# Kernel tuning notes

Hardware: AMD Instinct MI355X
Metric: run time of the kernel (lower is better)

The kernel has to match this reference:

```python
import jax, jax.numpy as jnp
import numpy as np

N = 65536          # number of points
K = 32             # max neighbors (padded)
C_IN = 64
C_OUT = 64
KERNEL = 27        # spatial filter bins (3x3x3)
MULT = 1           # depth multiplier
BN_EPS = 1e-5


def setup_inputs() -> dict:
    key = jax.random.key(0)
    ks = jax.random.split(key, 8)
    inputs = jax.random.normal(ks[0], (N, C_IN), dtype=jnp.float32)
    nn_count = jnp.maximum(jax.random.randint(ks[1], (N,), 0, K, dtype=jnp.int32), 1)
    nn_index = jax.random.randint(ks[2], (N, K), 0, N, dtype=jnp.int32)
    filt_index = jax.random.randint(ks[3], (N, K), 0, KERNEL, dtype=jnp.int32)
    # learned parameters (xavier-normal-ish init)
    sw_std = float(np.sqrt(2.0 / (KERNEL * C_IN + MULT)))
    spatial_weights = jax.random.normal(ks[4], (KERNEL, C_IN, MULT), dtype=jnp.float32) * sw_std
    dw_std = float(np.sqrt(2.0 / (C_IN * MULT + C_OUT)))
    depth_weights = jax.random.normal(ks[5], (C_IN * MULT, C_OUT), dtype=jnp.float32) * dw_std
    biases = jnp.zeros((1, C_OUT), dtype=jnp.float32)
    gamma = jnp.ones((C_OUT,), dtype=jnp.float32)
    beta = jnp.zeros((C_OUT,), dtype=jnp.float32)
    return {"inputs": inputs, "spatial_weights": spatial_weights,
            "depth_weights": depth_weights, "biases": biases,
            "gamma": gamma, "beta": beta,
            "nn_count": nn_count, "nn_index": nn_index, "filt_index": filt_index}


def reference(inputs, spatial_weights, depth_weights, biases, gamma, beta,
              nn_count, nn_index, filt_index):
    n, k = nn_index.shape
    # valid-neighbor mask for padded neighborhoods
    mask = (jnp.arange(k, dtype=jnp.int32)[None, :] < nn_count[:, None]).astype(inputs.dtype)  # [N,K]
    gathered = inputs[nn_index] * mask[:, :, None]            # [N,K,C]
    wg = spatial_weights[filt_index]                          # [N,K,C,M]
    # spatial filtering: average over valid neighbors with per-pair filter weights
    sp = jnp.einsum('nkc,nkcm->ncm', gathered, wg) / nn_count[:, None, None].astype(inputs.dtype)
    x = sp.reshape(n, -1) @ depth_weights + biases            # [N,C_OUT]
    x = jax.nn.relu(x)
    # BatchNorm1d (training mode: batch statistics, biased variance)
    mean = jnp.mean(x, axis=0)
    var = jnp.var(x, axis=0)
    out = gamma * (x - mean) * jax.lax.rsqrt(var + BN_EPS) + beta
    return out
```

## Files before the change

### kernel.cpp

```cpp
#include <hip/hip_runtime.h>
#include <math.h>

#define KMAX   32
#define CIN    64
#define COUT   64
#define NKERN  27
#define GPW    8
#define MMT    2
constexpr float BN_EPS = 1e-5f;

typedef _Float16 f16;
typedef _Float16 f16x2 __attribute__((ext_vector_type(2)));
typedef _Float16 f16x8 __attribute__((ext_vector_type(8)));
typedef float    f32x4 __attribute__((ext_vector_type(4)));

union h2i { f16x2 h; int i; };

__global__ __launch_bounds__(256) void k_cvtpack(
    const float* __restrict__ in,
    f16*         __restrict__ out,
    const float* __restrict__ dw,
    f16*         __restrict__ dwf,
    float*       __restrict__ stats,
    const int*   __restrict__ nn_count,
    const int*   __restrict__ nn_index,
    const int*   __restrict__ filt_index,
    int*         __restrict__ packed,
    float*       __restrict__ invc,
    int total4, int cvtBlocks, int total_q, int zrowIdx)
{
    const int bid = blockIdx.x;
    if (bid == 0) {
        const int t = threadIdx.x;
        if (t < 128) stats[t] = 0.0f;
        if (t < CIN) out[(size_t)zrowIdx * CIN + t] = (f16)0.0f;
        for (int i = t; i < 512; i += 256) {
            const int j = i >> 7, s = (i >> 6) & 1, l = i & 63;
            const int col = j * 16 + (l & 15);
            const int k0  = s * 32 + ((l >> 4) * 8);
            #pragma unroll
            for (int e = 0; e < 8; ++e)
                dwf[(size_t)i * 8 + e] = (f16)dw[(k0 + e) * COUT + col];
        }
    }
    if (bid < cvtBlocks) {
        const int stride = cvtBlocks * 256;
        for (int i = bid * 256 + threadIdx.x; i < total4; i += stride) {
            const float4 v = ((const float4*)in)[i];
            f16x2 a = { (f16)v.x, (f16)v.y };
            f16x2 b = { (f16)v.z, (f16)v.w };
            uint2 u;
            u.x = *(const unsigned int*)&a;
            u.y = *(const unsigned int*)&b;
            ((uint2*)out)[i] = u;
        }
    } else {
        const int t = (bid - cvtBlocks) * 256 + threadIdx.x;
        if (t < total_q) {
            const int n = t >> 3, q = t & 7;
            const int cnt = nn_count[n];
            const int4 ni = ((const int4*)nn_index)[t];
            const int4 fi = ((const int4*)filt_index)[t];
            const int k0 = q * 4;
            const int px = (((k0 + 0) < cnt ? ni.x : zrowIdx) << 7) | (fi.x << 25);
            const int py = (((k0 + 1) < cnt ? ni.y : zrowIdx) << 7) | (fi.y << 25);
            const int pz = (((k0 + 2) < cnt ? ni.z : zrowIdx) << 7) | (fi.z << 25);
            const int pw = (((k0 + 3) < cnt ? ni.w : zrowIdx) << 7) | (fi.w << 25);
            int* bp = packed + (size_t)n * KMAX;
            int2 ev = { px, pz };
            int2 od = { py, pw };
            *(int2*)(bp + 2 * q)      = ev;
            *(int2*)(bp + 16 + 2 * q) = od;
            if (q == 0) invc[n] = 1.0f / (float)cnt;
        }
    }
}

__global__ __launch_bounds__(256, 8) void k_gather(
    const f16*   __restrict__ gh,
    const float* __restrict__ sw,
    const int*   __restrict__ packed,
    const float* __restrict__ invc,
    f16*         __restrict__ sp)
{
    __shared__ f16 sw_lds[NKERN * CIN];
    const int tid = threadIdx.x;
    for (int i = tid; i < NKERN * CIN; i += 256) sw_lds[i] = (f16)sw[i];
    __syncthreads();

    const int wave = tid >> 6;
    const int lane = tid & 63;
    const int h    = lane >> 5;
    const unsigned cpos4 = (unsigned)(lane & 31) * 4;
    const int base = blockIdx.x * (4 * GPW) + wave * GPW;
    const char* __restrict__ ghb = (const char*)gh;
    const char* __restrict__ swb = (const char*)sw_lds;

    for (int p = 0; p < GPW; ++p) {
        const int n = base + p;
        const int4* __restrict__ pk4 =
            (const int4*)(packed + (size_t)n * KMAX + h * 16);

        int mypk[16];
        #pragma unroll
        for (int q = 0; q < 4; ++q) *(int4*)&mypk[4 * q] = pk4[q];
        const float ic = invc[n];

        f16x2 g2[16];
        #pragma unroll
        for (int i = 0; i < 16; ++i)
            g2[i] = *(const f16x2*)(ghb + (((unsigned)mypk[i] & 0xFFFFFFu) + cpos4));

        f16x2 a0 = {(f16)0.f, (f16)0.f}, a1 = a0, a2 = a0, a3 = a0;
        #pragma unroll
        for (int i = 0; i < 16; ++i) {
            const unsigned swoff = (((unsigned)mypk[i] >> 25) << 7) + cpos4;
            const f16x2 w2 = *(const f16x2*)(swb + swoff);
            f16x2& a = (i & 3) == 0 ? a0 : (i & 3) == 1 ? a1
                     : (i & 3) == 2 ? a2 : a3;
            a = __builtin_elementwise_fma(g2[i], w2, a);
        }
        f16x2 stot = (a0 + a1) + (a2 + a3);

        h2i cv; cv.h = stot;
        h2i ov; ov.i = __shfl_xor(cv.i, 32);
        stot = stot + ov.h;

        if (h == 0) {
            f16x2 res = { (f16)((float)stot.x * ic), (f16)((float)stot.y * ic) };
            *(f16x2*)(sp + (size_t)n * CIN + (cpos4 >> 1)) = res;
        }
    }
}

#define MM_LOAD_AB(r0)                                                        \
    const f16* arow = sp + (size_t)((r0) + (lane & 15)) * CIN + ((lane >> 4) * 8); \
    const f16x8 a0 = *(const f16x8*)(arow);                                   \
    const f16x8 a1 = *(const f16x8*)(arow + 32);

__global__ __launch_bounds__(256) void k_mm_stats(
    const f16*   __restrict__ sp,
    const f16*   __restrict__ dwf,
    const float* __restrict__ bias,
    float*       __restrict__ stats)
{
    __shared__ float rsum[4][4][16], rsq[4][4][16];
    const int tid = threadIdx.x;
    const int wave = tid >> 6, lane = tid & 63;

    const f16x8* dwf8 = (const f16x8*)dwf;
    f16x8 b[4][2];
    #pragma unroll
    for (int j = 0; j < 4; ++j) {
        b[j][0] = dwf8[(j * 2 + 0) * 64 + lane];
        b[j][1] = dwf8[(j * 2 + 1) * 64 + lane];
    }
    float bias_c[4];
    #pragma unroll
    for (int j = 0; j < 4; ++j) bias_c[j] = bias[j * 16 + (lane & 15)];

    float sum[4] = {0, 0, 0, 0}, sq[4] = {0, 0, 0, 0};
    const int rowbase = (blockIdx.x * 4 + wave) * (MMT * 16);

    for (int t = 0; t < MMT; ++t) {
        MM_LOAD_AB(rowbase + t * 16)
        #pragma unroll
        for (int j = 0; j < 4; ++j) {
            f32x4 acc = {0.f, 0.f, 0.f, 0.f};
            acc = __builtin_amdgcn_mfma_f32_16x16x32_f16(a0, b[j][0], acc, 0, 0, 0);
            acc = __builtin_amdgcn_mfma_f32_16x16x32_f16(a1, b[j][1], acc, 0, 0, 0);
            #pragma unroll
            for (int r = 0; r < 4; ++r) {
                const float x = fmaxf(acc[r] + bias_c[j], 0.0f);
                sum[j] += x;
                sq[j]  += x * x;
            }
        }
    }

    #pragma unroll
    for (int j = 0; j < 4; ++j) {
        sum[j] += __shfl_xor(sum[j], 16); sum[j] += __shfl_xor(sum[j], 32);
        sq[j]  += __shfl_xor(sq[j], 16);  sq[j]  += __shfl_xor(sq[j], 32);
    }
    if (lane < 16) {
        #pragma unroll
        for (int j = 0; j < 4; ++j) {
            rsum[wave][j][lane] = sum[j];
            rsq[wave][j][lane]  = sq[j];
        }
    }
    __syncthreads();
    if (wave == 0 && lane < 16) {
        #pragma unroll
        for (int j = 0; j < 4; ++j) {
            const float s = rsum[0][j][lane] + rsum[1][j][lane]
                          + rsum[2][j][lane] + rsum[3][j][lane];
            const float q = rsq[0][j][lane] + rsq[1][j][lane]
                          + rsq[2][j][lane] + rsq[3][j][lane];
            atomicAdd(&stats[j * 16 + lane], s);
            atomicAdd(&stats[COUT + j * 16 + lane], q);
        }
    }
}

__global__ void k_finalize(const float* __restrict__ stats,
                           const float* __restrict__ gamma,
                           const float* __restrict__ beta,
                           float* __restrict__ sc_sh, float invN) {
    const int j = threadIdx.x;
    const float mean = stats[j] * invN;
    const float var  = stats[COUT + j] * invN - mean * mean;
    const float s    = gamma[j] * rsqrtf(var + BN_EPS);
    sc_sh[j]        = s;
    sc_sh[COUT + j] = beta[j] - mean * s;
}

__global__ __launch_bounds__(256) void k_mm_out(
    const f16*   __restrict__ sp,
    const f16*   __restrict__ dwf,
    const float* __restrict__ bias,
    const float* __restrict__ sc_sh,
    float*       __restrict__ out)
{
    const int tid = threadIdx.x;
    const int wave = tid >> 6, lane = tid & 63;

    const f16x8* dwf8 = (const f16x8*)dwf;
    f16x8 b[4][2];
    #pragma unroll
    for (int j = 0; j < 4; ++j) {
        b[j][0] = dwf8[(j * 2 + 0) * 64 + lane];
        b[j][1] = dwf8[(j * 2 + 1) * 64 + lane];
    }
    float bias_c[4], sc[4], sh[4];
    #pragma unroll
    for (int j = 0; j < 4; ++j) {
        const int c = j * 16 + (lane & 15);
        bias_c[j] = bias[c];
        sc[j]     = sc_sh[c];
        sh[j]     = sc_sh[COUT + c];
    }

    const int rowbase = (blockIdx.x * 4 + wave) * (MMT * 16);
    for (int t = 0; t < MMT; ++t) {
        const int r0 = rowbase + t * 16;
        MM_LOAD_AB(r0)
        #pragma unroll
        for (int j = 0; j < 4; ++j) {
            f32x4 acc = {0.f, 0.f, 0.f, 0.f};
            acc = __builtin_amdgcn_mfma_f32_16x16x32_f16(a0, b[j][0], acc, 0, 0, 0);
            acc = __builtin_amdgcn_mfma_f32_16x16x32_f16(a1, b[j][1], acc, 0, 0, 0);
            #pragma unroll
            for (int r = 0; r < 4; ++r) {
                const float x = fmaxf(acc[r] + bias_c[j], 0.0f);
                out[(size_t)(r0 + (lane >> 4) * 4 + r) * COUT + j * 16 + (lane & 15)]
                    = fmaf(x, sc[j], sh[j]);
            }
        }
    }
}

extern "C" void kernel_launch(void* const* d_in, const int* in_sizes, int n_in,
                              void* d_out, int out_size, void* d_ws, size_t ws_size,
                              hipStream_t stream) {
    const float* inputs     = (const float*)d_in[0];
    const float* sw         = (const float*)d_in[1];
    const float* dw         = (const float*)d_in[2];
    const float* bias       = (const float*)d_in[3];
    const float* gamma      = (const float*)d_in[4];
    const float* beta       = (const float*)d_in[5];
    const int*   nn_count   = (const int*)d_in[6];
    const int*   nn_index   = (const int*)d_in[7];
    const int*   filt_index = (const int*)d_in[8];

    const int N = in_sizes[0] / CIN;
    float* out   = (float*)d_out;

    float* stats  = (float*)d_ws;
    float* sc_sh  = (float*)d_ws + 128;
    f16*   in_h   = (f16*)((float*)d_ws + 256);
    f16*   spb    = in_h + (size_t)(N + 1) * CIN;
    f16*   dwf    = spb + (size_t)N * CIN;
    int*   packed = (int*)(dwf + 4096);
    float* invc   = (float*)(packed + (size_t)N * KMAX);

    const int total4    = N * CIN / 4;
    const int cvtBlocks = 2048;
    const int total_q   = N * (KMAX / 4);
    const int packBlocks = (total_q + 255) / 256;

    k_cvtpack<<<cvtBlocks + packBlocks, 256, 0, stream>>>(
        inputs, in_h, dw, dwf, stats,
        nn_count, nn_index, filt_index, packed, invc,
        total4, cvtBlocks, total_q, N);

    k_gather<<<N / (4 * GPW), 256, 0, stream>>>(in_h, sw, packed, invc, spb);

    k_mm_stats<<<N / (4 * MMT * 16), 256, 0, stream>>>(spb, dwf, bias, stats);
    k_finalize<<<1, COUT, 0, stream>>>(stats, gamma, beta, sc_sh, 1.0f / (float)N);
    k_mm_out<<<N / (4 * MMT * 16), 256, 0, stream>>>(spb, dwf, bias, sc_sh, out);
}
```

Measured before the change: 59.76 us.

## Fuse matmul-stats, BN finalize and output into one cooperative kernel

Result: slower. 119.2 us (+99.5%).

```diff
diff --git a/kernel.cpp b/kernel.cpp
--- a/kernel.cpp
+++ b/kernel.cpp
@@ -1,5 +1,8 @@
 #include <hip/hip_runtime.h>
+#include <hip/hip_cooperative_groups.h>
 #include <math.h>
+
+namespace cg = cooperative_groups;
 
 #define KMAX   32
 #define CIN    64
@@ -138,11 +141,15 @@
     const f16x8 a0 = *(const f16x8*)(arow);                                   \
     const f16x8 a1 = *(const f16x8*)(arow + 32);
 
-__global__ __launch_bounds__(256) void k_mm_stats(
+__global__ __launch_bounds__(256, 4) void k_mm_fused(
     const f16*   __restrict__ sp,
     const f16*   __restrict__ dwf,
     const float* __restrict__ bias,
-    float*       __restrict__ stats)
+    const float* __restrict__ gamma,
+    const float* __restrict__ beta,
+    float*       __restrict__ stats,
+    float*       __restrict__ out,
+    float invN)
 {
     __shared__ float rsum[4][4][16], rsq[4][4][16];
     const int tid = threadIdx.x;
@@ -159,9 +166,11 @@
     #pragma unroll
     for (int j = 0; j < 4; ++j) bias_c[j] = bias[j * 16 + (lane & 15)];
 
+    float xv[MMT][4][4];
     float sum[4] = {0, 0, 0, 0}, sq[4] = {0, 0, 0, 0};
     const int rowbase = (blockIdx.x * 4 + wave) * (MMT * 16);
 
+    #pragma unroll
     for (int t = 0; t < MMT; ++t) {
         MM_LOAD_AB(rowbase + t * 16)
         #pragma unroll
@@ -172,6 +181,7 @@
             #pragma unroll
             for (int r = 0; r < 4; ++r) {
                 const float x = fmaxf(acc[r] + bias_c[j], 0.0f);
+                xv[t][j][r] = x;
                 sum[j] += x;
                 sq[j]  += x * x;
             }
@@ -202,60 +212,30 @@
             atomicAdd(&stats[COUT + j * 16 + lane], q);
         }
     }
-}
-
-__global__ void k_finalize(const float* __restrict__ stats,
-                           const float* __restrict__ gamma,
-                           const float* __restrict__ beta,
-                           float* __restrict__ sc_sh, float invN) {
-    const int j = threadIdx.x;
-    const float mean = stats[j] * invN;
-    const float var  = stats[COUT + j] * invN - mean * mean;
-    const float s    = gamma[j] * rsqrtf(var + BN_EPS);
-    sc_sh[j]        = s;
-    sc_sh[COUT + j] = beta[j] - mean * s;
-}
-
-__global__ __launch_bounds__(256) void k_mm_out(
-    const f16*   __restrict__ sp,
-    const f16*   __restrict__ dwf,
-    const float* __restrict__ bias,
-    const float* __restrict__ sc_sh,
-    float*       __restrict__ out)
-{
-    const int tid = threadIdx.x;
-    const int wave = tid >> 6, lane = tid & 63;
-
-    const f16x8* dwf8 = (const f16x8*)dwf;
-    f16x8 b[4][2];
-    #pragma unroll
-    for (int j = 0; j < 4; ++j) {
-        b[j][0] = dwf8[(j * 2 + 0) * 64 + lane];
-        b[j][1] = dwf8[(j * 2 + 1) * 64 + lane];
-    }
-    float bias_c[4], sc[4], sh[4];
+
+    __threadfence();
+    cg::this_grid().sync();
+
+    float sc[4], sh[4];
     #pragma unroll
     for (int j = 0; j < 4; ++j) {
         const int c = j * 16 + (lane & 15);
-        bias_c[j] = bias[c];
-        sc[j]     = sc_sh[c];
-        sh[j]     = sc_sh[COUT + c];
-    }
-
-    const int rowbase = (blockIdx.x * 4 + wave) * (MMT * 16);
+        const float mean = stats[c] * invN;
+        const float var  = stats[COUT + c] * invN - mean * mean;
+        const float s    = gamma[c] * rsqrtf(var + BN_EPS);
+        sc[j] = s;
+        sh[j] = beta[c] - mean * s;
+    }
+
+    #pragma unroll
     for (int t = 0; t < MMT; ++t) {
         const int r0 = rowbase + t * 16;
-        MM_LOAD_AB(r0)
-        #pragma unroll
-        for (int j = 0; j < 4; ++j) {
-            f32x4 acc = {0.f, 0.f, 0.f, 0.f};
-            acc = __builtin_amdgcn_mfma_f32_16x16x32_f16(a0, b[j][0], acc, 0, 0, 0);
-            acc = __builtin_amdgcn_mfma_f32_16x16x32_f16(a1, b[j][1], acc, 0, 0, 0);
+        #pragma unroll
+        for (int j = 0; j < 4; ++j) {
             #pragma unroll
             for (int r = 0; r < 4; ++r) {
-                const float x = fmaxf(acc[r] + bias_c[j], 0.0f);
                 out[(size_t)(r0 + (lane >> 4) * 4 + r) * COUT + j * 16 + (lane & 15)]
-                    = fmaf(x, sc[j], sh[j]);
+                    = fmaf(xv[t][j][r], sc[j], sh[j]);
             }
         }
     }
@@ -278,7 +258,6 @@
     float* out   = (float*)d_out;
 
     float* stats  = (float*)d_ws;
-    float* sc_sh  = (float*)d_ws + 128;
     f16*   in_h   = (f16*)((float*)d_ws + 256);
     f16*   spb    = in_h + (size_t)(N + 1) * CIN;
     f16*   dwf    = spb + (size_t)N * CIN;
@@ -297,7 +276,12 @@
 
     k_gather<<<N / (4 * GPW), 256, 0, stream>>>(in_h, sw, packed, invc, spb);
 
-    k_mm_stats<<<N / (4 * MMT * 16), 256, 0, stream>>>(spb, dwf, bias, stats);
-    k_finalize<<<1, COUT, 0, stream>>>(stats, gamma, beta, sc_sh, 1.0f / (float)N);
-    k_mm_out<<<N / (4 * MMT * 16), 256, 0, stream>>>(spb, dwf, bias, sc_sh, out);
-}
+    const f16* sp_c    = spb;
+    const f16* dwf_c   = dwf;
+    float invN = 1.0f / (float)N;
+    void* args[] = { (void*)&sp_c, (void*)&dwf_c, (void*)&bias, (void*)&gamma,
+                     (void*)&beta, (void*)&stats, (void*)&out, (void*)&invN };
+    hipLaunchCooperativeKernel((const void*)k_mm_fused,
+                               dim3(N / (4 * MMT * 16)), dim3(256),
+                               args, 0, stream);
+}
```
